# Optimization experiments

Measured on AMD Instinct MI355X. Metric: run time of the kernel, lower is better.

Reference implementation:

```python
import jax, jax.numpy as jnp
import numpy as np

N, H, E = 8192, 2048, 8  # tokens, hidden_size, num_experts


def setup_inputs() -> dict:
    key = jax.random.key(0)
    ks = jax.random.split(key, 5)
    s = 1.0 / np.sqrt(H)  # torch nn.Linear default init scale
    return {
        "x": jax.random.normal(ks[0], (N, H), dtype=jnp.float32),
        "W": jax.random.uniform(ks[1], (E, H, H), jnp.float32, -s, s),   # per-expert dense weight (out,in)->einsum form
        "b": jax.random.uniform(ks[2], (E, H), jnp.float32, -s, s),
        "Wg": jax.random.uniform(ks[3], (H, E), jnp.float32, -s, s),     # gate Linear
        "bg": jax.random.uniform(ks[4], (E,), jnp.float32, -s, s),
        "cached": jnp.zeros((E, H), jnp.float32),  # kv_caches[i].get_all() at init (zero buffers)
    }


def reference(x, W, b, Wg, bg, cached):
    # gate_probs = softmax(gate(x))                       [N, E]
    gate = jax.nn.softmax(x @ Wg + bg, axis=-1)
    # all experts batched: relu(x @ W_i + b_i)            [E, N, H]
    h = jax.nn.relu(jnp.einsum('nh,ehf->enf', x, W) + b[:, None, :])
    # + cached_values.detach() per expert (zero-init buffers, stop-gradient)
    h = h + jax.lax.stop_gradient(cached)[:, None, :]
    # sum_i gate[:, i] * h_i                              [N, H]
    return jnp.einsum('ne,enh->nh', gate, h)
```

## Files before the change

### kernel.cpp

```cpp
#include <hip/hip_runtime.h>


#define NT 8192
#define HD 2048
#define NE 8

typedef __attribute__((ext_vector_type(8))) short short8;
typedef __attribute__((ext_vector_type(4))) float f32x4;

__device__ __forceinline__ unsigned int f2bf(float f) {
  unsigned int u = __float_as_uint(f);
  u += 0x7FFFu + ((u >> 16) & 1u);
  return u >> 16;
}

__global__ void gate_kernel(const float* __restrict__ x, const float* __restrict__ Wg,
                            const float* __restrict__ bg, float* __restrict__ gate) {
  const int w = threadIdx.x >> 6, l = threadIdx.x & 63;
  const int n = blockIdx.x * 4 + w;
  const float4* x4 = (const float4*)(x + (size_t)n * HD);
  const float4* wg4 = (const float4*)Wg;
  float acc[NE] = {0.f, 0.f, 0.f, 0.f, 0.f, 0.f, 0.f, 0.f};
  #pragma unroll
  for (int i = 0; i < HD / 256; ++i) {
    const int h4 = l + 64 * i;
    const float4 xv = x4[h4];
    #pragma unroll
    for (int c = 0; c < 4; ++c) {
      const float xs = (c == 0) ? xv.x : (c == 1) ? xv.y : (c == 2) ? xv.z : xv.w;
      const float4 w0 = wg4[(h4 * 4 + c) * 2];
      const float4 w1 = wg4[(h4 * 4 + c) * 2 + 1];
      acc[0] += xs * w0.x; acc[1] += xs * w0.y; acc[2] += xs * w0.z; acc[3] += xs * w0.w;
      acc[4] += xs * w1.x; acc[5] += xs * w1.y; acc[6] += xs * w1.z; acc[7] += xs * w1.w;
    }
  }
  #pragma unroll
  for (int off = 32; off > 0; off >>= 1) {
    #pragma unroll
    for (int e = 0; e < NE; ++e) acc[e] += __shfl_xor(acc[e], off);
  }
  if (l == 0) {
    float lg[NE], m = -1e30f;
    #pragma unroll
    for (int e = 0; e < NE; ++e) { lg[e] = acc[e] + bg[e]; m = fmaxf(m, lg[e]); }
    float s = 0.f;
    #pragma unroll
    for (int e = 0; e < NE; ++e) { lg[e] = expf(lg[e] - m); s += lg[e]; }
    const float inv = 1.f / s;
    #pragma unroll
    for (int e = 0; e < NE; ++e) gate[(size_t)n * NE + e] = lg[e] * inv;
  }
}

__global__ void xconv_kernel(const float* __restrict__ x, unsigned short* __restrict__ xb) {
  const size_t i = (size_t)blockIdx.x * 256 + threadIdx.x;
  const float4 a = ((const float4*)x)[i * 2];
  const float4 c = ((const float4*)x)[i * 2 + 1];
  uint4 o;
  o.x = f2bf(a.x) | (f2bf(a.y) << 16);
  o.y = f2bf(a.z) | (f2bf(a.w) << 16);
  o.z = f2bf(c.x) | (f2bf(c.y) << 16);
  o.w = f2bf(c.z) | (f2bf(c.w) << 16);
  ((uint4*)xb)[i] = o;
}

__global__ void wtrans_kernel(const float* __restrict__ W, unsigned short* __restrict__ Wt) {
  __shared__ unsigned short tl[64][65];
  const int e = blockIdx.z, kb = blockIdx.y * 64, fb = blockIdx.x * 64;
  const int c = threadIdx.x & 63, rq = threadIdx.x >> 6;
  const float* Wp = W + (size_t)e * HD * HD;
  #pragma unroll
  for (int i = 0; i < 16; ++i) {
    const int r = rq * 16 + i;
    tl[r][c] = (unsigned short)f2bf(Wp[(size_t)(kb + r) * HD + fb + c]);
  }
  __syncthreads();
  unsigned short* Wtp = Wt + (size_t)e * HD * HD;
  #pragma unroll
  for (int i = 0; i < 16; ++i) {
    const int fr = rq * 16 + i;
    Wtp[(size_t)(fb + fr) * HD + kb + c] = tl[c][fr];
  }
}

__global__ __launch_bounds__(256, 2) void moe_main(
    const unsigned short* __restrict__ xb, const unsigned short* __restrict__ wt,
    const float* __restrict__ b, const float* __restrict__ cached,
    const float* __restrict__ gate, float* __restrict__ out) {
  __shared__ unsigned short lds[8192];
  auto lds3 = (__attribute__((address_space(3))) unsigned short*)lds;

  const int t = threadIdx.x, w = t >> 6, l = t & 63;
  const int wm = w >> 1, wn = w & 1;
  const int n0 = blockIdx.y * 128, f0 = blockIdx.x * 128;

  const int sr = l >> 2;
  const int chl = (l & 3) ^ ((l >> 3) & 3);
  const unsigned short* aSrc = xb + (size_t)n0 * HD + chl * 8;

  const int fm = l & 15;
  const int qr = l >> 4;
  const int rg = qr ^ ((l >> 1) & 3);
  const unsigned short* aRd = &lds[(size_t)(wm * 64 + fm) * 32 + rg * 8];
  const unsigned short* bRd = &lds[4096 + (size_t)(wn * 64 + fm) * 32 + rg * 8];

  f32x4 oacc[4][4] = {};

  for (int e = 0; e < NE; ++e) {
    f32x4 acc[4][4] = {};
    const unsigned short* bSrc = wt + (size_t)e * HD * HD + (size_t)f0 * HD + chl * 8;

    for (int kt = 0; kt < HD / 32; ++kt) {
      __syncthreads();
      #pragma unroll
      for (int j = 0; j < 2; ++j) {
        const int rw = (w * 2 + j) * 16 + sr;
        __builtin_amdgcn_global_load_lds(
            (const __attribute__((address_space(1))) void*)(aSrc + (size_t)rw * HD + kt * 32),
            (__attribute__((address_space(3))) void*)(lds3 + (w * 2 + j) * 512), 16, 0, 0);
        __builtin_amdgcn_global_load_lds(
            (const __attribute__((address_space(1))) void*)(bSrc + (size_t)rw * HD + kt * 32),
            (__attribute__((address_space(3))) void*)(lds3 + 4096 + (w * 2 + j) * 512), 16, 0, 0);
      }
      __syncthreads();

      short8 av[4], bv[4];
      #pragma unroll
      for (int mi = 0; mi < 4; ++mi) av[mi] = *(const short8*)(aRd + mi * 512);
      #pragma unroll
      for (int ni = 0; ni < 4; ++ni) bv[ni] = *(const short8*)(bRd + ni * 512);
      #pragma unroll
      for (int mi = 0; mi < 4; ++mi)
        #pragma unroll
        for (int ni = 0; ni < 4; ++ni)
          acc[mi][ni] = __builtin_amdgcn_mfma_f32_16x16x32_bf16(av[mi], bv[ni], acc[mi][ni], 0, 0, 0);
    }

    float gv[16];
    #pragma unroll
    for (int mi = 0; mi < 4; ++mi)
      #pragma unroll
      for (int j2 = 0; j2 < 4; ++j2)
        gv[mi * 4 + j2] = gate[(size_t)(n0 + wm * 64 + mi * 16 + qr * 4 + j2) * NE + e];
    #pragma unroll
    for (int ni = 0; ni < 4; ++ni) {
      const int f = f0 + wn * 64 + ni * 16 + fm;
      const float bias = b[(size_t)e * HD + f];
      const float cv = cached[(size_t)e * HD + f];
      #pragma unroll
      for (int mi = 0; mi < 4; ++mi)
        #pragma unroll
        for (int j2 = 0; j2 < 4; ++j2) {
          float v = acc[mi][ni][j2] + bias;
          v = fmaxf(v, 0.f) + cv;
          oacc[mi][ni][j2] += gv[mi * 4 + j2] * v;
        }
    }
  }

  #pragma unroll
  for (int mi = 0; mi < 4; ++mi)
    #pragma unroll
    for (int j2 = 0; j2 < 4; ++j2) {
      const size_t n = n0 + wm * 64 + mi * 16 + qr * 4 + j2;
      float* orow = out + n * HD + f0 + wn * 64 + fm;
      #pragma unroll
      for (int ni = 0; ni < 4; ++ni) orow[ni * 16] = oacc[mi][ni][j2];
    }
}

extern "C" void kernel_launch(void* const* d_in, const int* in_sizes, int n_in,
                              void* d_out, int out_size, void* d_ws, size_t ws_size,
                              hipStream_t stream) {
  const float* x      = (const float*)d_in[0];
  const float* W      = (const float*)d_in[1];
  const float* b      = (const float*)d_in[2];
  const float* Wg     = (const float*)d_in[3];
  const float* bg     = (const float*)d_in[4];
  const float* cached = (const float*)d_in[5];
  float* out = (float*)d_out;

  char* ws = (char*)d_ws;
  float* gate = (float*)ws;
  unsigned short* xbuf = (unsigned short*)(ws + (size_t)NT * NE * 4);
  unsigned short* wtb  = (unsigned short*)(ws + (size_t)NT * NE * 4 + (size_t)NT * HD * 2);

  gate_kernel<<<NT / 4, 256, 0, stream>>>(x, Wg, bg, gate);
  xconv_kernel<<<(NT * HD / 8) / 256, 256, 0, stream>>>(x, xbuf);
  wtrans_kernel<<<dim3(HD / 64, HD / 64, NE), 256, 0, stream>>>(W, wtb);
  moe_main<<<dim3(HD / 128, NT / 128), 256, 0, stream>>>(xbuf, wtb, b, cached, gate, out);
}
```

Measured before the change: 970.6 us.

## Triple-buffer LDS with larger 128x256 tiles, K=64 stages, and fused x conversion

Rewrites the main MoE GEMM to use 512-thread blocks computing 128x256 output tiles. K advances in 64-wide stages through a triple-buffered dynamic LDS ring, prefetching two stages ahead with async global-to-LDS loads, manual vmcnt waits, split barriers, and s_setprio around the MFMA bursts. The aim is to hide global load latency and raise data reuse per LDS byte. The separate fp32-to-bf16 conversion of x is folded into the gate kernel, removing one launch and one extra read of x. In exchange it needs 144KB of LDS per block, which caps occupancy at one block per CU, and it depends on hand-tuned wait counts being exactly right.

```diff
diff --git a/kernel.cpp b/kernel.cpp
--- a/kernel.cpp
+++ b/kernel.cpp
@@ -15,16 +15,22 @@
 }
 
 __global__ void gate_kernel(const float* __restrict__ x, const float* __restrict__ Wg,
-                            const float* __restrict__ bg, float* __restrict__ gate) {
+                            const float* __restrict__ bg, float* __restrict__ gate,
+                            unsigned short* __restrict__ xb) {
   const int w = threadIdx.x >> 6, l = threadIdx.x & 63;
   const int n = blockIdx.x * 4 + w;
   const float4* x4 = (const float4*)(x + (size_t)n * HD);
+  uint2* xbrow = (uint2*)(xb + (size_t)n * HD);
   const float4* wg4 = (const float4*)Wg;
   float acc[NE] = {0.f, 0.f, 0.f, 0.f, 0.f, 0.f, 0.f, 0.f};
   #pragma unroll
   for (int i = 0; i < HD / 256; ++i) {
     const int h4 = l + 64 * i;
     const float4 xv = x4[h4];
+    uint2 o;
+    o.x = f2bf(xv.x) | (f2bf(xv.y) << 16);
+    o.y = f2bf(xv.z) | (f2bf(xv.w) << 16);
+    xbrow[h4] = o;
     #pragma unroll
     for (int c = 0; c < 4; ++c) {
       const float xs = (c == 0) ? xv.x : (c == 1) ? xv.y : (c == 2) ? xv.z : xv.w;
@@ -52,18 +58,6 @@
   }
 }
 
-__global__ void xconv_kernel(const float* __restrict__ x, unsigned short* __restrict__ xb) {
-  const size_t i = (size_t)blockIdx.x * 256 + threadIdx.x;
-  const float4 a = ((const float4*)x)[i * 2];
-  const float4 c = ((const float4*)x)[i * 2 + 1];
-  uint4 o;
-  o.x = f2bf(a.x) | (f2bf(a.y) << 16);
-  o.y = f2bf(a.z) | (f2bf(a.w) << 16);
-  o.z = f2bf(c.x) | (f2bf(c.y) << 16);
-  o.w = f2bf(c.z) | (f2bf(c.w) << 16);
-  ((uint4*)xb)[i] = o;
-}
-
 __global__ void wtrans_kernel(const float* __restrict__ W, unsigned short* __restrict__ Wt) {
   __shared__ unsigned short tl[64][65];
   const int e = blockIdx.z, kb = blockIdx.y * 64, fb = blockIdx.x * 64;
@@ -83,57 +77,103 @@
   }
 }
 
-__global__ __launch_bounds__(256, 2) void moe_main(
+__global__ __launch_bounds__(512, 2) void moe_main(
     const unsigned short* __restrict__ xb, const unsigned short* __restrict__ wt,
     const float* __restrict__ b, const float* __restrict__ cached,
     const float* __restrict__ gate, float* __restrict__ out) {
-  __shared__ unsigned short lds[8192];
+  extern __shared__ unsigned short lds[];
   auto lds3 = (__attribute__((address_space(3))) unsigned short*)lds;
 
   const int t = threadIdx.x, w = t >> 6, l = t & 63;
-  const int wm = w >> 1, wn = w & 1;
-  const int n0 = blockIdx.y * 128, f0 = blockIdx.x * 128;
-
-  const int sr = l >> 2;
-  const int chl = (l & 3) ^ ((l >> 3) & 3);
-  const unsigned short* aSrc = xb + (size_t)n0 * HD + chl * 8;
-
-  const int fm = l & 15;
-  const int qr = l >> 4;
-  const int rg = qr ^ ((l >> 1) & 3);
-  const unsigned short* aRd = &lds[(size_t)(wm * 64 + fm) * 32 + rg * 8];
-  const unsigned short* bRd = &lds[4096 + (size_t)(wn * 64 + fm) * 32 + rg * 8];
+  const int wm = w >> 2, wn = w & 3;
+  const int n0 = (blockIdx.x >> 3) * 128;
+  const int f0 = (blockIdx.x & 7) * 256;
+
+  const int sr = l >> 3;
+  const int cl = (l & 7) ^ sr;
+  const unsigned short* aB0 = xb + (size_t)(n0 + (2 * w + 0) * 8 + sr) * HD + cl * 8;
+  const unsigned short* aB1 = xb + (size_t)(n0 + (2 * w + 1) * 8 + sr) * HD + cl * 8;
+  const unsigned short* bB0 = wt + (size_t)(f0 + (4 * w + 0) * 8 + sr) * HD + cl * 8;
+  const unsigned short* bB1 = wt + (size_t)(f0 + (4 * w + 1) * 8 + sr) * HD + cl * 8;
+  const unsigned short* bB2 = wt + (size_t)(f0 + (4 * w + 2) * 8 + sr) * HD + cl * 8;
+  const unsigned short* bB3 = wt + (size_t)(f0 + (4 * w + 3) * 8 + sr) * HD + cl * 8;
+
+  const int fm = l & 15, qr = l >> 4;
+  const int aOff = (wm * 64 + fm) * 64;
+  const int bOff = 8192 + (wn * 64 + fm) * 64;
+  const int ch0 = ((0 + qr) ^ (fm & 7)) * 8;
+  const int ch1 = ((4 + qr) ^ (fm & 7)) * 8;
+
+  #define GLD(src, dstoff) __builtin_amdgcn_global_load_lds( \
+      (const __attribute__((address_space(1))) void*)(src),  \
+      (__attribute__((address_space(3))) void*)(lds3 + (dstoff)), 16, 0, 0)
+
+  #pragma unroll
+  for (int T0 = 0; T0 < 2; ++T0) {
+    const size_t ko = (size_t)(T0 & 31) * 64;
+    const size_t eo = ko;
+    const int base = (T0 % 3) * 24576;
+    GLD(aB0 + ko, base + (2 * w + 0) * 512);
+    GLD(aB1 + ko, base + (2 * w + 1) * 512);
+    GLD(bB0 + eo, base + 8192 + (4 * w + 0) * 512);
+    GLD(bB1 + eo, base + 8192 + (4 * w + 1) * 512);
+    GLD(bB2 + eo, base + 8192 + (4 * w + 2) * 512);
+    GLD(bB3 + eo, base + 8192 + (4 * w + 3) * 512);
+  }
 
   f32x4 oacc[4][4] = {};
 
   for (int e = 0; e < NE; ++e) {
     f32x4 acc[4][4] = {};
-    const unsigned short* bSrc = wt + (size_t)e * HD * HD + (size_t)f0 * HD + chl * 8;
-
-    for (int kt = 0; kt < HD / 32; ++kt) {
-      __syncthreads();
-      #pragma unroll
-      for (int j = 0; j < 2; ++j) {
-        const int rw = (w * 2 + j) * 16 + sr;
-        __builtin_amdgcn_global_load_lds(
-            (const __attribute__((address_space(1))) void*)(aSrc + (size_t)rw * HD + kt * 32),
-            (__attribute__((address_space(3))) void*)(lds3 + (w * 2 + j) * 512), 16, 0, 0);
-        __builtin_amdgcn_global_load_lds(
-            (const __attribute__((address_space(1))) void*)(bSrc + (size_t)rw * HD + kt * 32),
-            (__attribute__((address_space(3))) void*)(lds3 + 4096 + (w * 2 + j) * 512), 16, 0, 0);
+    for (int kt = 0; kt < 32; ++kt) {
+      const int T = e * 32 + kt;
+      if (T == 255) { asm volatile("s_waitcnt vmcnt(0)" ::: "memory"); }
+      else          { asm volatile("s_waitcnt vmcnt(6)" ::: "memory"); }
+      __builtin_amdgcn_s_barrier();
+
+      const unsigned short* buf = lds + (T % 3) * 24576;
+      const bool doStage = (T + 2) < 256;
+      const int Ts = T + 2;
+      const int sbase = (Ts % 3) * 24576;
+      const size_t ko = (size_t)(Ts & 31) * 64;
+      const size_t eo = (size_t)(Ts >> 5) * HD * HD + ko;
+
+      #pragma unroll
+      for (int ph = 0; ph < 4; ++ph) {
+        if (ph == 0 && doStage) {
+          GLD(aB0 + ko, sbase + (2 * w + 0) * 512);
+          GLD(aB1 + ko, sbase + (2 * w + 1) * 512);
+        }
+        if (ph == 1 && doStage) {
+          GLD(bB0 + eo, sbase + 8192 + (4 * w + 0) * 512);
+          GLD(bB1 + eo, sbase + 8192 + (4 * w + 1) * 512);
+        }
+        if (ph == 2 && doStage) { GLD(bB2 + eo, sbase + 8192 + (4 * w + 2) * 512); }
+        if (ph == 3 && doStage) { GLD(bB3 + eo, sbase + 8192 + (4 * w + 3) * 512); }
+
+        const int pm = ph >> 1, pn = ph & 1;
+        short8 a0k0 = *(const short8*)(buf + aOff + (pm * 2 + 0) * 1024 + ch0);
+        short8 a0k1 = *(const short8*)(buf + aOff + (pm * 2 + 0) * 1024 + ch1);
+        short8 a1k0 = *(const short8*)(buf + aOff + (pm * 2 + 1) * 1024 + ch0);
+        short8 a1k1 = *(const short8*)(buf + aOff + (pm * 2 + 1) * 1024 + ch1);
+        short8 b0k0 = *(const short8*)(buf + bOff + (pn * 2 + 0) * 1024 + ch0);
+        short8 b0k1 = *(const short8*)(buf + bOff + (pn * 2 + 0) * 1024 + ch1);
+        short8 b1k0 = *(const short8*)(buf + bOff + (pn * 2 + 1) * 1024 + ch0);
+        short8 b1k1 = *(const short8*)(buf + bOff + (pn * 2 + 1) * 1024 + ch1);
+
+        __builtin_amdgcn_s_barrier();
+        __builtin_amdgcn_s_setprio(1);
+        acc[pm*2+0][pn*2+0] = __builtin_amdgcn_mfma_f32_16x16x32_bf16(a0k0, b0k0, acc[pm*2+0][pn*2+0], 0, 0, 0);
+        acc[pm*2+0][pn*2+1] = __builtin_amdgcn_mfma_f32_16x16x32_bf16(a0k0, b1k0, acc[pm*2+0][pn*2+1], 0, 0, 0);
+        acc[pm*2+1][pn*2+0] = __builtin_amdgcn_mfma_f32_16x16x32_bf16(a1k0, b0k0, acc[pm*2+1][pn*2+0], 0, 0, 0);
+        acc[pm*2+1][pn*2+1] = __builtin_amdgcn_mfma_f32_16x16x32_bf16(a1k0, b1k0, acc[pm*2+1][pn*2+1], 0, 0, 0);
+        acc[pm*2+0][pn*2+0] = __builtin_amdgcn_mfma_f32_16x16x32_bf16(a0k1, b0k1, acc[pm*2+0][pn*2+0], 0, 0, 0);
+        acc[pm*2+0][pn*2+1] = __builtin_amdgcn_mfma_f32_16x16x32_bf16(a0k1, b1k1, acc[pm*2+0][pn*2+1], 0, 0, 0);
+        acc[pm*2+1][pn*2+0] = __builtin_amdgcn_mfma_f32_16x16x32_bf16(a1k1, b0k1, acc[pm*2+1][pn*2+0], 0, 0, 0);
+        acc[pm*2+1][pn*2+1] = __builtin_amdgcn_mfma_f32_16x16x32_bf16(a1k1, b1k1, acc[pm*2+1][pn*2+1], 0, 0, 0);
+        __builtin_amdgcn_s_setprio(0);
+        __builtin_amdgcn_s_barrier();
       }
-      __syncthreads();
-
-      short8 av[4], bv[4];
-      #pragma unroll
-      for (int mi = 0; mi < 4; ++mi) av[mi] = *(const short8*)(aRd + mi * 512);
-      #pragma unroll
-      for (int ni = 0; ni < 4; ++ni) bv[ni] = *(const short8*)(bRd + ni * 512);
-      #pragma unroll
-      for (int mi = 0; mi < 4; ++mi)
-        #pragma unroll
-        for (int ni = 0; ni < 4; ++ni)
-          acc[mi][ni] = __builtin_amdgcn_mfma_f32_16x16x32_bf16(av[mi], bv[ni], acc[mi][ni], 0, 0, 0);
     }
 
     float gv[16];
@@ -167,6 +207,7 @@
       #pragma unroll
       for (int ni = 0; ni < 4; ++ni) orow[ni * 16] = oacc[mi][ni][j2];
     }
+  #undef GLD
 }
 
 extern "C" void kernel_launch(void* const* d_in, const int* in_sizes, int n_in,
@@ -185,8 +226,10 @@
   unsigned short* xbuf = (unsigned short*)(ws + (size_t)NT * NE * 4);
   unsigned short* wtb  = (unsigned short*)(ws + (size_t)NT * NE * 4 + (size_t)NT * HD * 2);
 
-  gate_kernel<<<NT / 4, 256, 0, stream>>>(x, Wg, bg, gate);
-  xconv_kernel<<<(NT * HD / 8) / 256, 256, 0, stream>>>(x, xbuf);
+  (void)hipFuncSetAttribute((const void*)moe_main,
+                            hipFuncAttributeMaxDynamicSharedMemorySize, 147456);
+
+  gate_kernel<<<NT / 4, 256, 0, stream>>>(x, Wg, bg, gate, xbuf);
   wtrans_kernel<<<dim3(HD / 64, HD / 64, NE), 256, 0, stream>>>(W, wtb);
-  moe_main<<<dim3(HD / 128, NT / 128), 256, 0, stream>>>(xbuf, wtb, b, cached, gate, out);
-}
+  moe_main<<<dim3((NT / 128) * (HD / 256)), 512, 147456, stream>>>(xbuf, wtb, b, cached, gate, out);
+}
```

Measured after the change: 946.7 us. 1.03x faster.
